# Performance work log

Measured on AMD Instinct MI355X. Metric: run time of the kernel, lower is better.

Reference implementation:

```python
import jax, jax.numpy as jnp
import numpy as np

B, S, D, H = 2, 2048, 1024, 16
HD = D // H


def setup_inputs() -> dict:
    key = jax.random.key(0)
    ks = jax.random.split(key, 12)
    s = 0.02
    inp = {
        "query": jax.random.normal(ks[0], (B, S, D), dtype=jnp.float32),
        "Wq": jax.random.normal(ks[1], (D, D), dtype=jnp.float32) * s,
        "bq": jnp.zeros((D,), jnp.float32),
        "Wk": jax.random.normal(ks[2], (D, D), dtype=jnp.float32) * s,
        "bk": jnp.zeros((D,), jnp.float32),
        "Wv": jax.random.normal(ks[3], (D, D), dtype=jnp.float32) * s,
        "bv": jnp.zeros((D,), jnp.float32),
        "Wo": jax.random.normal(ks[4], (D, D), dtype=jnp.float32) * s,
        "bo": jnp.zeros((D,), jnp.float32),
        "Wm1": jax.random.normal(ks[5], (D // 4, D), dtype=jnp.float32) * s,
        "bm1": jnp.zeros((D // 4,), jnp.float32),
        "Wm2": jax.random.normal(ks[6], (D, D // 4), dtype=jnp.float32) * s,
        "bm2": jnp.zeros((D,), jnp.float32),
        "dopamine": jnp.ones((1,), jnp.float32),
        "serotonin": jnp.ones((1,), jnp.float32),
        "norepinephrine": jnp.ones((1,), jnp.float32),
        "acetylcholine": jnp.ones((1,), jnp.float32),
        "attention_scale": jnp.ones((1,), jnp.float32),
        "attention_bias": jnp.zeros((1,), jnp.float32),
    }
    return inp


def reference(query, Wq, bq, Wk, bk, Wv, bv, Wo, bo, Wm1, bm1, Wm2, bm2,
              dopamine, serotonin, norepinephrine, acetylcholine,
              attention_scale, attention_bias):
    b, s, d = query.shape
    scale = HD ** -0.5
    split = lambda t: t.reshape(b, s, H, HD).transpose(0, 2, 1, 3)  # [b,h,s,hd]
    q = split(query @ Wq.T + bq)
    k = split(query @ Wk.T + bk)
    v = split(query @ Wv.T + bv)
    scores = jnp.einsum('bhqd,bhkd->bhqk', q, k) * scale
    w = jax.nn.softmax(scores, axis=-1)  # dropout=0 (eval)
    attn = jnp.einsum('bhqk,bhkd->bhqd', w, v)
    # neuromodulation MLP on flattened query, then combined scalar gate
    mod = jax.nn.relu(query @ Wm1.T + bm1) @ Wm2.T + bm2  # [b,s,d]
    gate = (dopamine + serotonin + norepinephrine + acetylcholine) / 4.0  # [1]
    neuro = split(mod * gate)  # [b,h,s,hd]
    attn = (attn * attention_scale + attention_bias) * (1.0 + neuro)
    out = attn.transpose(0, 2, 1, 3).reshape(b, s, d) @ Wo.T + bo
    return out
```

## Files before the change

### kernel.cpp

```cpp
#include <hip/hip_runtime.h>
#include <hip/hip_bf16.h>
#include <stdint.h>
#include <math.h>


typedef __attribute__((ext_vector_type(8))) short short8;
typedef __attribute__((ext_vector_type(8))) unsigned short ushort8;
typedef __attribute__((ext_vector_type(4))) float floatx4;

#define MFMA16(a, b, c) __builtin_amdgcn_mfma_f32_16x16x32_bf16(a, b, c, 0, 0, 0)

__device__ __forceinline__ unsigned short f2bf(float f) {
    union { float f; uint32_t u; } v; v.f = f;
    uint32_t r = v.u + 0x7fffu + ((v.u >> 16) & 1u);
    return (unsigned short)(r >> 16);
}
__device__ __forceinline__ float bf2f(unsigned short s) {
    union { uint32_t u; float f; } v; v.u = ((uint32_t)s) << 16;
    return v.f;
}
__device__ __forceinline__ uint32_t pk2(float a, float b) {
    __hip_bfloat162 t = __float22bfloat162_rn(make_float2(a, b));
    uint32_t u; __builtin_memcpy(&u, &t, 4); return u;
}

typedef const __attribute__((address_space(1))) void gvoid_t;
typedef __attribute__((address_space(3))) void lvoid_t;
__device__ __forceinline__ void gld16(const void* g, void* l) {
    __builtin_amdgcn_global_load_lds((gvoid_t*)g, (lvoid_t*)l, 16, 0, 0);
}

template<int BN, bool OUTBF>
__device__ __forceinline__ void gemm_core(const unsigned short* __restrict__ A,
                                          const unsigned short* __restrict__ W,
                                          const float* __restrict__ bias,
                                          void* __restrict__ C,
                                          int N, int K, int bm, int bn,
                                          bool relu, float osc,
                                          unsigned short* __restrict__ vt)
{
    constexpr int MT = (BN == 128) ? 4 : 2;
    constexpr int SU = (BN == 128) ? 4 : 3;
    __shared__ __align__(16) unsigned short As[2][128][32];
    __shared__ __align__(16) unsigned short Ws[2][BN][32];

    const int tid  = threadIdx.x;
    const int w    = tid >> 6, lane = tid & 63;
    const int ln   = lane & 15, quad = lane >> 4;
    const int wm   = (BN == 128) ? (w >> 1) * 64 : w * 32;
    const int wn   = (BN == 128) ? (w & 1) * 64 : 0;

    floatx4 acc[MT][4] = {};

    auto stage = [&](int k0, int bb) {
        #pragma unroll
        for (int i = 0; i < SU; i++) {
            const int t = w * SU + i;
            if (t < 8) {
                const int r0  = t * 16;
                const int row = r0 + (lane >> 2);
                const int c   = (lane & 3) ^ ((row >> 1) & 3);
                gld16(&A[(size_t)(bm + row) * K + k0 + c * 8], &As[bb][r0][0]);
            } else if (t < 8 + BN / 16) {
                const int r0  = (t - 8) * 16;
                const int row = r0 + (lane >> 2);
                const int c   = (lane & 3) ^ ((row >> 1) & 3);
                gld16(&W[(size_t)(bn + row) * K + k0 + c * 8], &Ws[bb][r0][0]);
            }
        }
    };

    stage(0, 0);

    const int KI = K >> 5;
    for (int ki = 0; ki < KI; ki++) {
        const int bb = ki & 1;
        __syncthreads();
        if (ki + 1 < KI) stage((ki + 1) << 5, bb ^ 1);

        short8 af[MT], bf[4];
        #pragma unroll
        for (int mt = 0; mt < MT; mt++) {
            const int row = wm + mt * 16 + ln;
            af[mt] = *(const short8*)&As[bb][row][(quad ^ ((row >> 1) & 3)) * 8];
        }
        #pragma unroll
        for (int nt = 0; nt < 4; nt++) {
            const int row = wn + nt * 16 + ln;
            bf[nt] = *(const short8*)&Ws[bb][row][(quad ^ ((row >> 1) & 3)) * 8];
        }
        #pragma unroll
        for (int mt = 0; mt < MT; mt++)
            #pragma unroll
            for (int nt = 0; nt < 4; nt++)
                acc[mt][nt] = MFMA16(af[mt], bf[nt], acc[mt][nt]);
    }

    float bv[4];
    #pragma unroll
    for (int nt = 0; nt < 4; nt++) bv[nt] = bias[bn + wn + nt * 16 + ln];

    if (vt != nullptr) {
        #pragma unroll
        for (int mt = 0; mt < MT; mt++) {
            const int rowg = bm + wm + mt * 16 + quad * 4;
            const int b = rowg >> 11, s = rowg & 2047;
            #pragma unroll
            for (int nt = 0; nt < 4; nt++) {
                const int n = bn + wn + nt * 16 + ln;
                const int h = n >> 6, hd = n & 63;
                float v0 = acc[mt][nt][0] + bv[nt];
                float v1 = acc[mt][nt][1] + bv[nt];
                float v2 = acc[mt][nt][2] + bv[nt];
                float v3 = acc[mt][nt][3] + bv[nt];
                uint2 pk; pk.x = pk2(v0, v1); pk.y = pk2(v2, v3);
                *(uint2*)&vt[((size_t)(b * 16 + h) * 64 + hd) * 2048 + s] = pk;
            }
        }
        return;
    }

    #pragma unroll
    for (int mt = 0; mt < MT; mt++) {
        #pragma unroll
        for (int nt = 0; nt < 4; nt++) {
            #pragma unroll
            for (int r = 0; r < 4; r++) {
                float v = (acc[mt][nt][r] + bv[nt]) * osc;
                if (relu) v = fmaxf(v, 0.f);
                const size_t row = (size_t)bm + wm + mt * 16 + quad * 4 + r;
                const size_t col = (size_t)bn + wn + nt * 16 + ln;
                if (OUTBF) ((unsigned short*)C)[row * N + col] = f2bf(v);
                else       ((float*)C)[row * N + col] = v;
            }
        }
    }
}

#define QSCALE (0.125f * 1.44269504088896f)

__global__ __launch_bounds__(256) void qkv_mlp1_gemm(
    const unsigned short* __restrict__ A,
    const unsigned short* __restrict__ Wq, const unsigned short* __restrict__ Wk,
    const unsigned short* __restrict__ Wv, const unsigned short* __restrict__ Wm1,
    const float* __restrict__ bq, const float* __restrict__ bk,
    const float* __restrict__ bv, const float* __restrict__ bm1,
    unsigned short* __restrict__ Qo, unsigned short* __restrict__ Ko,
    unsigned short* __restrict__ Vt, unsigned short* __restrict__ Ho)
{
    const int flat = blockIdx.x + 26 * blockIdx.y;
    const int g = flat & 7, s = flat >> 3;
    const int bx = (g & 1) * 13 + (s % 13);
    const int bm = ((g >> 1) * 8 + (s / 13)) * 128;

    const unsigned short* W; const float* bias; unsigned short* C = nullptr;
    unsigned short* vt = nullptr;
    int N, bn; bool relu = false; float osc = 1.f;
    if (bx < 8)       { W = Wq;  bias = bq;  C = Qo; N = 1024; bn = bx * 128; osc = QSCALE; }
    else if (bx < 16) { W = Wk;  bias = bk;  C = Ko; N = 1024; bn = (bx - 8) * 128; }
    else if (bx < 24) { W = Wv;  bias = bv;  vt = Vt; N = 1024; bn = (bx - 16) * 128; }
    else              { W = Wm1; bias = bm1; C = Ho; N = 256;  bn = (bx - 24) * 128; relu = true; }
    gemm_core<128, true>(A, W, bias, C, N, 1024, bm, bn, relu, osc, vt);
}

template<bool OUTBF>
__global__ __launch_bounds__(256) void gemm_bn64(const unsigned short* __restrict__ A,
                                                 const unsigned short* __restrict__ W,
                                                 const float* __restrict__ bias,
                                                 void* __restrict__ C, int N, int K)
{
    const int flat = blockIdx.x + 16 * blockIdx.y;
    const int g = flat & 7, s = flat >> 3;
    const int bx = (g & 1) * 8 + (s & 7);
    const int bm = ((g >> 1) * 8 + (s >> 3)) * 128;
    gemm_core<64, OUTBF>(A, W, bias, C, N, K, bm, bx * 64, false, 1.f, nullptr);
}

__global__ __launch_bounds__(256) void attn_mfma(const unsigned short* __restrict__ Qg,
                                                 const unsigned short* __restrict__ Kg,
                                                 const unsigned short* __restrict__ Vtg,
                                                 const unsigned short* __restrict__ Modg,
                                                 unsigned short* __restrict__ Yg,
                                                 const float* __restrict__ dop,
                                                 const float* __restrict__ ser,
                                                 const float* __restrict__ nor,
                                                 const float* __restrict__ ach,
                                                 const float* __restrict__ asc,
                                                 const float* __restrict__ abi)
{
    __shared__ __align__(16) unsigned short Ks[2][128][64];
    __shared__ __align__(16) unsigned short Vs[2][64][128];
    __shared__ __align__(16) unsigned short Ps[4][2][16][64];

    const int tid = threadIdx.x;
    const int w   = tid >> 6, lane = tid & 63;
    const int ln  = lane & 15, quad = lane >> 4;
    const int h   = blockIdx.x, qt = blockIdx.y, b = blockIdx.z;

    const size_t kbase = (size_t)b * 2048 * 1024 + h * 64;
    const size_t vbase = (size_t)(b * 16 + h) * 64 * 2048;

    const size_t qrowbase = (size_t)b * 2048 + qt * 128 + w * 32;
    short8 qf[2][2];
    #pragma unroll
    for (int q2 = 0; q2 < 2; q2++) {
        const unsigned short* qp = Qg + (qrowbase + q2 * 16 + ln) * 1024 + h * 64;
        qf[q2][0] = *(const short8*)&qp[quad * 8];
        qf[q2][1] = *(const short8*)&qp[32 + quad * 8];
    }

    floatx4 o[2][4] = {};
    float lsum[2] = {0.f, 0.f};

    auto stage = [&](int kc, int bb) {
        #pragma unroll
        for (int i = 0; i < 8; i++) {
            const int t = w * 8 + i;
            if (t < 16) {
                const int R = t * 8 + (lane >> 3);
                const int c = (lane & 7) ^ (R & 7);
                gld16(&Kg[kbase + (size_t)(kc * 128 + R) * 1024 + c * 8], &Ks[bb][t * 8][0]);
            } else {
                const int tv = t - 16;
                const int R  = tv * 4 + (lane >> 4);
                const int c  = (lane & 15) ^ (R & 15);
                gld16(&Vtg[vbase + (size_t)R * 2048 + kc * 128 + c * 8], &Vs[bb][tv * 4][0]);
            }
        }
    };

    stage(0, 0);

    for (int kc = 0; kc < 16; kc++) {
        const int bb = kc & 1;
        __syncthreads();
        if (kc + 1 < 16) stage(kc + 1, bb ^ 1);

        #pragma unroll
        for (int half = 0; half < 2; half++) {
            short8 kf[4][2];
            #pragma unroll
            for (int mt = 0; mt < 4; mt++) {
                const int row = half * 64 + mt * 16 + ln;
                kf[mt][0] = *(const short8*)&Ks[bb][row][((0 + quad) ^ (ln & 7)) * 8];
                kf[mt][1] = *(const short8*)&Ks[bb][row][((4 + quad) ^ (ln & 7)) * 8];
            }

            #pragma unroll
            for (int q2 = 0; q2 < 2; q2++) {
                floatx4 sc[4];
                #pragma unroll
                for (int mt = 0; mt < 4; mt++) {
                    floatx4 z = {};
                    z = MFMA16(kf[mt][0], qf[q2][0], z);
                    z = MFMA16(kf[mt][1], qf[q2][1], z);
                    sc[mt] = z;
                }
                #pragma unroll
                for (int mt = 0; mt < 4; mt++) {
                    const float p0 = __builtin_amdgcn_exp2f(sc[mt][0]);
                    const float p1 = __builtin_amdgcn_exp2f(sc[mt][1]);
                    const float p2 = __builtin_amdgcn_exp2f(sc[mt][2]);
                    const float p3 = __builtin_amdgcn_exp2f(sc[mt][3]);
                    lsum[q2] += (p0 + p1) + (p2 + p3);
                    uint2 pk; pk.x = pk2(p0, p1); pk.y = pk2(p2, p3);
                    const int c2 = (mt * 2 + (quad >> 1)) ^ (ln & 7);
                    *(uint2*)((char*)&Ps[w][q2][ln][0] + c2 * 16 + (quad & 1) * 8) = pk;
                }
            }

            short8 pf[2][2];
            #pragma unroll
            for (int q2 = 0; q2 < 2; q2++)
                #pragma unroll
                for (int ks = 0; ks < 2; ks++) {
                    const int c2 = (ks * 4 + quad) ^ (ln & 7);
                    pf[q2][ks] = *(const short8*)((char*)&Ps[w][q2][ln][0] + c2 * 16);
                }
            #pragma unroll
            for (int ntv = 0; ntv < 4; ntv++) {
                const int vrow = ntv * 16 + ln;
                #pragma unroll
                for (int ks = 0; ks < 2; ks++) {
                    const int c2 = (half * 8 + ks * 4 + quad) ^ (ln & 15);
                    const short8 vf = *(const short8*)&Vs[bb][vrow][c2 * 8];
                    o[0][ntv] = MFMA16(pf[0][ks], vf, o[0][ntv]);
                    o[1][ntv] = MFMA16(pf[1][ks], vf, o[1][ntv]);
                }
            }
        }
    }

    #pragma unroll
    for (int q2 = 0; q2 < 2; q2++) {
        float s = lsum[q2];
        s += __shfl_xor(s, 16);
        s += __shfl_xor(s, 32);
        lsum[q2] = s;
    }

    const float gate = 0.25f * (dop[0] + ser[0] + nor[0] + ach[0]);
    const float scb = asc[0], bib = abi[0];
    #pragma unroll
    for (int q2 = 0; q2 < 2; q2++) {
        #pragma unroll
        for (int r = 0; r < 4; r++) {
            const float inv = 1.f / __shfl(lsum[q2], quad * 4 + r);
            const size_t row = qrowbase + q2 * 16 + quad * 4 + r;
            #pragma unroll
            for (int ntv = 0; ntv < 4; ntv++) {
                const size_t col = (size_t)h * 64 + ntv * 16 + ln;
                const float x  = o[q2][ntv][r] * inv;
                const float mo = bf2f(Modg[row * 1024 + col]);
                const float y  = (x * scb + bib) * (1.f + mo * gate);
                Yg[row * 1024 + col] = f2bf(y);
            }
        }
    }
}

__global__ __launch_bounds__(256) void fused_cast(
    const float* __restrict__ q,   const float* __restrict__ wq,
    const float* __restrict__ wk,  const float* __restrict__ wv,
    const float* __restrict__ wo,  const float* __restrict__ wm1,
    const float* __restrict__ wm2,
    unsigned short* __restrict__ dq,  unsigned short* __restrict__ dwq,
    unsigned short* __restrict__ dwk, unsigned short* __restrict__ dwv,
    unsigned short* __restrict__ dwo, unsigned short* __restrict__ dwm1,
    unsigned short* __restrict__ dwm2)
{
    const size_t u = (size_t)blockIdx.x * 256 + threadIdx.x;
    const float* src; unsigned short* dst; size_t off;
    if      (u <  524288) { src = q;   dst = dq;   off = u; }
    else if (u <  655360) { src = wq;  dst = dwq;  off = u - 524288; }
    else if (u <  786432) { src = wk;  dst = dwk;  off = u - 655360; }
    else if (u <  917504) { src = wv;  dst = dwv;  off = u - 786432; }
    else if (u < 1048576) { src = wo;  dst = dwo;  off = u - 917504; }
    else if (u < 1081344) { src = wm1; dst = dwm1; off = u - 1048576; }
    else                  { src = wm2; dst = dwm2; off = u - 1081344; }
    const float4* p = (const float4*)src + off * 2;
    const float4 a = p[0], c = p[1];
    uint4 o;
    o.x = pk2(a.x, a.y); o.y = pk2(a.z, a.w);
    o.z = pk2(c.x, c.y); o.w = pk2(c.z, c.w);
    *(uint4*)&dst[off * 8] = o;
}

extern "C" void kernel_launch(void* const* d_in, const int* in_sizes, int n_in,
                              void* d_out, int out_size, void* d_ws, size_t ws_size,
                              hipStream_t stream)
{
    const float* query = (const float*)d_in[0];
    const float* Wq  = (const float*)d_in[1];
    const float* bq  = (const float*)d_in[2];
    const float* Wk  = (const float*)d_in[3];
    const float* bk  = (const float*)d_in[4];
    const float* Wv  = (const float*)d_in[5];
    const float* bv  = (const float*)d_in[6];
    const float* Wo  = (const float*)d_in[7];
    const float* bo  = (const float*)d_in[8];
    const float* Wm1 = (const float*)d_in[9];
    const float* bm1 = (const float*)d_in[10];
    const float* Wm2 = (const float*)d_in[11];
    const float* bm2 = (const float*)d_in[12];
    const float* dop = (const float*)d_in[13];
    const float* ser = (const float*)d_in[14];
    const float* nor = (const float*)d_in[15];
    const float* ach = (const float*)d_in[16];
    const float* asc = (const float*)d_in[17];
    const float* abi = (const float*)d_in[18];

    char* ws = (char*)d_ws;
    const size_t MB = 1024 * 1024;
    unsigned short* Qry  = (unsigned short*)(ws);
    unsigned short* Wqb  = (unsigned short*)(ws + 8 * MB);
    unsigned short* Wkb  = (unsigned short*)(ws + 10 * MB);
    unsigned short* Wvb  = (unsigned short*)(ws + 12 * MB);
    unsigned short* Wob  = (unsigned short*)(ws + 14 * MB);
    unsigned short* Wm1b = (unsigned short*)(ws + 16 * MB);
    unsigned short* Wm2b = (unsigned short*)(ws + 16 * MB + 512 * 1024);
    unsigned short* Qb   = (unsigned short*)(ws + 17 * MB);
    unsigned short* Kb   = (unsigned short*)(ws + 25 * MB);
    unsigned short* Modb = (unsigned short*)(ws + 33 * MB);
    unsigned short* Vt   = (unsigned short*)(ws + 41 * MB);
    unsigned short* Yb   = (unsigned short*)(ws + 49 * MB);
    unsigned short* Hm   = (unsigned short*)(ws + 57 * MB);

    fused_cast<<<4352, 256, 0, stream>>>(query, Wq, Wk, Wv, Wo, Wm1, Wm2,
                                         Qry, Wqb, Wkb, Wvb, Wob, Wm1b, Wm2b);

    qkv_mlp1_gemm<<<dim3(26, 32), 256, 0, stream>>>(
        Qry, Wqb, Wkb, Wvb, Wm1b, bq, bk, bv, bm1, Qb, Kb, Vt, Hm);

    gemm_bn64<true><<<dim3(16, 32), 256, 0, stream>>>(Hm, Wm2b, bm2, (void*)Modb, 1024, 256);

    attn_mfma<<<dim3(16, 16, 2), 256, 0, stream>>>(Qb, Kb, Vt, Modb, Yb,
                                                   dop, ser, nor, ach, asc, abi);

    gemm_bn64<false><<<dim3(16, 32), 256, 0, stream>>>(Yb, Wob, bo, d_out, 1024, 1024);
}
```

Measured before the change: 235.7 us.

## Use BK=64 tiles for the BN=64 GEMMs and compute softmax row sums with MFMA

Splits the shared GEMM core into a 128-wide version and a separate 64-wide version. The 64-wide version, used for the output and MLP2 projections, now stages 64-element K slices with an 8-way XOR swizzle, which halves the number of K iterations and barriers. In attention, the per-lane exp-sum accumulation and its cross-lane shuffles are replaced by an MFMA of the bf16 probabilities against a ones vector. That sum uses the bf16-rounded P, so it matches what is multiplied with V, but it adds MFMA work in the inner loop. The larger LDS tiles may lower occupancy.

```diff
diff --git a/kernel.cpp b/kernel.cpp
--- a/kernel.cpp
+++ b/kernel.cpp
@@ -30,38 +30,35 @@
     __builtin_amdgcn_global_load_lds((gvoid_t*)g, (lvoid_t*)l, 16, 0, 0);
 }
 
-template<int BN, bool OUTBF>
-__device__ __forceinline__ void gemm_core(const unsigned short* __restrict__ A,
-                                          const unsigned short* __restrict__ W,
-                                          const float* __restrict__ bias,
-                                          void* __restrict__ C,
-                                          int N, int K, int bm, int bn,
-                                          bool relu, float osc,
-                                          unsigned short* __restrict__ vt)
-{
-    constexpr int MT = (BN == 128) ? 4 : 2;
-    constexpr int SU = (BN == 128) ? 4 : 3;
+template<bool OUTBF>
+__device__ __forceinline__ void gemm_core128(const unsigned short* __restrict__ A,
+                                             const unsigned short* __restrict__ W,
+                                             const float* __restrict__ bias,
+                                             void* __restrict__ C,
+                                             int N, int K, int bm, int bn,
+                                             bool relu, float osc,
+                                             unsigned short* __restrict__ vt)
+{
     __shared__ __align__(16) unsigned short As[2][128][32];
-    __shared__ __align__(16) unsigned short Ws[2][BN][32];
+    __shared__ __align__(16) unsigned short Ws[2][128][32];
 
     const int tid  = threadIdx.x;
     const int w    = tid >> 6, lane = tid & 63;
     const int ln   = lane & 15, quad = lane >> 4;
-    const int wm   = (BN == 128) ? (w >> 1) * 64 : w * 32;
-    const int wn   = (BN == 128) ? (w & 1) * 64 : 0;
-
-    floatx4 acc[MT][4] = {};
+    const int wm   = (w >> 1) * 64, wn = (w & 1) * 64;
+
+    floatx4 acc[4][4] = {};
 
     auto stage = [&](int k0, int bb) {
         #pragma unroll
-        for (int i = 0; i < SU; i++) {
-            const int t = w * SU + i;
+        for (int i = 0; i < 4; i++) {
+            const int t = w * 4 + i;
             if (t < 8) {
                 const int r0  = t * 16;
                 const int row = r0 + (lane >> 2);
                 const int c   = (lane & 3) ^ ((row >> 1) & 3);
                 gld16(&A[(size_t)(bm + row) * K + k0 + c * 8], &As[bb][r0][0]);
-            } else if (t < 8 + BN / 16) {
+            } else {
                 const int r0  = (t - 8) * 16;
                 const int row = r0 + (lane >> 2);
                 const int c   = (lane & 3) ^ ((row >> 1) & 3);
@@ -78,9 +75,9 @@
         __syncthreads();
         if (ki + 1 < KI) stage((ki + 1) << 5, bb ^ 1);
 
-        short8 af[MT], bf[4];
-        #pragma unroll
-        for (int mt = 0; mt < MT; mt++) {
+        short8 af[4], bf[4];
+        #pragma unroll
+        for (int mt = 0; mt < 4; mt++) {
             const int row = wm + mt * 16 + ln;
             af[mt] = *(const short8*)&As[bb][row][(quad ^ ((row >> 1) & 3)) * 8];
         }
@@ -90,7 +87,7 @@
             bf[nt] = *(const short8*)&Ws[bb][row][(quad ^ ((row >> 1) & 3)) * 8];
         }
         #pragma unroll
-        for (int mt = 0; mt < MT; mt++)
+        for (int mt = 0; mt < 4; mt++)
             #pragma unroll
             for (int nt = 0; nt < 4; nt++)
                 acc[mt][nt] = MFMA16(af[mt], bf[nt], acc[mt][nt]);
@@ -102,18 +99,16 @@
 
     if (vt != nullptr) {
         #pragma unroll
-        for (int mt = 0; mt < MT; mt++) {
+        for (int mt = 0; mt < 4; mt++) {
             const int rowg = bm + wm + mt * 16 + quad * 4;
             const int b = rowg >> 11, s = rowg & 2047;
             #pragma unroll
             for (int nt = 0; nt < 4; nt++) {
                 const int n = bn + wn + nt * 16 + ln;
                 const int h = n >> 6, hd = n & 63;
-                float v0 = acc[mt][nt][0] + bv[nt];
-                float v1 = acc[mt][nt][1] + bv[nt];
-                float v2 = acc[mt][nt][2] + bv[nt];
-                float v3 = acc[mt][nt][3] + bv[nt];
-                uint2 pk; pk.x = pk2(v0, v1); pk.y = pk2(v2, v3);
+                uint2 pk;
+                pk.x = pk2(acc[mt][nt][0] + bv[nt], acc[mt][nt][1] + bv[nt]);
+                pk.y = pk2(acc[mt][nt][2] + bv[nt], acc[mt][nt][3] + bv[nt]);
                 *(uint2*)&vt[((size_t)(b * 16 + h) * 64 + hd) * 2048 + s] = pk;
             }
         }
@@ -121,7 +116,7 @@
     }
 
     #pragma unroll
-    for (int mt = 0; mt < MT; mt++) {
+    for (int mt = 0; mt < 4; mt++) {
         #pragma unroll
         for (int nt = 0; nt < 4; nt++) {
             #pragma unroll
@@ -130,6 +125,92 @@
                 if (relu) v = fmaxf(v, 0.f);
                 const size_t row = (size_t)bm + wm + mt * 16 + quad * 4 + r;
                 const size_t col = (size_t)bn + wn + nt * 16 + ln;
+                if (OUTBF) ((unsigned short*)C)[row * N + col] = f2bf(v);
+                else       ((float*)C)[row * N + col] = v;
+            }
+        }
+    }
+}
+
+template<bool OUTBF>
+__device__ __forceinline__ void gemm_core64(const unsigned short* __restrict__ A,
+                                            const unsigned short* __restrict__ W,
+                                            const float* __restrict__ bias,
+                                            void* __restrict__ C,
+                                            int N, int K, int bm, int bn)
+{
+    __shared__ __align__(16) unsigned short As[2][128][64];
+    __shared__ __align__(16) unsigned short Ws[2][64][64];
+
+    const int tid  = threadIdx.x;
+    const int w    = tid >> 6, lane = tid & 63;
+    const int ln   = lane & 15, quad = lane >> 4;
+    const int wm   = w * 32;
+
+    floatx4 acc[2][4] = {};
+
+    auto stage = [&](int k0, int bb) {
+        #pragma unroll
+        for (int i = 0; i < 6; i++) {
+            const int t = w * 6 + i;
+            if (t < 16) {
+                const int row = t * 8 + (lane >> 3);
+                const int c   = (lane & 7) ^ (row & 7);
+                gld16(&A[(size_t)(bm + row) * K + k0 + c * 8], &As[bb][t * 8][0]);
+            } else {
+                const int tv  = t - 16;
+                const int row = tv * 8 + (lane >> 3);
+                const int c   = (lane & 7) ^ (row & 7);
+                gld16(&W[(size_t)(bn + row) * K + k0 + c * 8], &Ws[bb][tv * 8][0]);
+            }
+        }
+    };
+
+    stage(0, 0);
+
+    const int KI = K >> 6;
+    for (int ki = 0; ki < KI; ki++) {
+        const int bb = ki & 1;
+        __syncthreads();
+        if (ki + 1 < KI) stage((ki + 1) << 6, bb ^ 1);
+
+        short8 af[2][2], bf[4][2];
+        #pragma unroll
+        for (int mt = 0; mt < 2; mt++) {
+            const int row = wm + mt * 16 + ln;
+            #pragma unroll
+            for (int s = 0; s < 2; s++)
+                af[mt][s] = *(const short8*)&As[bb][row][(((s * 4 + quad)) ^ (row & 7)) * 8];
+        }
+        #pragma unroll
+        for (int nt = 0; nt < 4; nt++) {
+            const int row = nt * 16 + ln;
+            #pragma unroll
+            for (int s = 0; s < 2; s++)
+                bf[nt][s] = *(const short8*)&Ws[bb][row][(((s * 4 + quad)) ^ (row & 7)) * 8];
+        }
+        #pragma unroll
+        for (int s = 0; s < 2; s++)
+            #pragma unroll
+            for (int mt = 0; mt < 2; mt++)
+                #pragma unroll
+                for (int nt = 0; nt < 4; nt++)
+                    acc[mt][nt] = MFMA16(af[mt][s], bf[nt][s], acc[mt][nt]);
+    }
+
+    float bv[4];
+    #pragma unroll
+    for (int nt = 0; nt < 4; nt++) bv[nt] = bias[bn + nt * 16 + ln];
+
+    #pragma unroll
+    for (int mt = 0; mt < 2; mt++) {
+        #pragma unroll
+        for (int nt = 0; nt < 4; nt++) {
+            #pragma unroll
+            for (int r = 0; r < 4; r++) {
+                const float v = acc[mt][nt][r] + bv[nt];
+                const size_t row = (size_t)bm + wm + mt * 16 + quad * 4 + r;
+                const size_t col = (size_t)bn + nt * 16 + ln;
                 if (OUTBF) ((unsigned short*)C)[row * N + col] = f2bf(v);
                 else       ((float*)C)[row * N + col] = v;
             }
@@ -160,7 +241,7 @@
     else if (bx < 16) { W = Wk;  bias = bk;  C = Ko; N = 1024; bn = (bx - 8) * 128; }
     else if (bx < 24) { W = Wv;  bias = bv;  vt = Vt; N = 1024; bn = (bx - 16) * 128; }
     else              { W = Wm1; bias = bm1; C = Ho; N = 256;  bn = (bx - 24) * 128; relu = true; }
-    gemm_core<128, true>(A, W, bias, C, N, 1024, bm, bn, relu, osc, vt);
+    gemm_core128<true>(A, W, bias, C, N, 1024, bm, bn, relu, osc, vt);
 }
 
 template<bool OUTBF>
@@ -173,8 +254,9 @@
     const int g = flat & 7, s = flat >> 3;
     const int bx = (g & 1) * 8 + (s & 7);
     const int bm = ((g >> 1) * 8 + (s >> 3)) * 128;
-    gemm_core<64, OUTBF>(A, W, bias, C, N, K, bm, bx * 64, false, 1.f, nullptr);
-}
+    gemm_core64<OUTBF>(A, W, bias, C, N, K, bm, bx * 64);
+}
+
 
 __global__ __launch_bounds__(256) void attn_mfma(const unsigned short* __restrict__ Qg,
                                                  const unsigned short* __restrict__ Kg,
@@ -209,8 +291,12 @@
         qf[q2][1] = *(const short8*)&qp[32 + quad * 8];
     }
 
+    short8 ones8;
+    #pragma unroll
+    for (int j = 0; j < 8; j++) ones8[j] = (short)0x3F80;
+
     floatx4 o[2][4] = {};
-    float lsum[2] = {0.f, 0.f};
+    floatx4 ls[2] = {};
 
     auto stage = [&](int kc, int bb) {
         #pragma unroll
@@ -262,7 +348,6 @@
                     const float p1 = __builtin_amdgcn_exp2f(sc[mt][1]);
                     const float p2 = __builtin_amdgcn_exp2f(sc[mt][2]);
                     const float p3 = __builtin_amdgcn_exp2f(sc[mt][3]);
-                    lsum[q2] += (p0 + p1) + (p2 + p3);
                     uint2 pk; pk.x = pk2(p0, p1); pk.y = pk2(p2, p3);
                     const int c2 = (mt * 2 + (quad >> 1)) ^ (ln & 7);
                     *(uint2*)((char*)&Ps[w][q2][ln][0] + c2 * 16 + (quad & 1) * 8) = pk;
@@ -277,6 +362,11 @@
                     const int c2 = (ks * 4 + quad) ^ (ln & 7);
                     pf[q2][ks] = *(const short8*)((char*)&Ps[w][q2][ln][0] + c2 * 16);
                 }
+            #pragma unroll
+            for (int q2 = 0; q2 < 2; q2++)
+                #pragma unroll
+                for (int ks = 0; ks < 2; ks++)
+                    ls[q2] = MFMA16(pf[q2][ks], ones8, ls[q2]);
             #pragma unroll
             for (int ntv = 0; ntv < 4; ntv++) {
                 const int vrow = ntv * 16 + ln;
@@ -291,21 +381,13 @@
         }
     }
 
-    #pragma unroll
-    for (int q2 = 0; q2 < 2; q2++) {
-        float s = lsum[q2];
-        s += __shfl_xor(s, 16);
-        s += __shfl_xor(s, 32);
-        lsum[q2] = s;
-    }
-
     const float gate = 0.25f * (dop[0] + ser[0] + nor[0] + ach[0]);
     const float scb = asc[0], bib = abi[0];
     #pragma unroll
     for (int q2 = 0; q2 < 2; q2++) {
         #pragma unroll
         for (int r = 0; r < 4; r++) {
-            const float inv = 1.f / __shfl(lsum[q2], quad * 4 + r);
+            const float inv = 1.f / ls[q2][r];
             const size_t row = qrowbase + q2 * 16 + quad * 4 + r;
             #pragma unroll
             for (int ntv = 0; ntv < 4; ntv++) {
```

After: 227.5 us. 1.04x faster.
